# Kernel tuning notes

Measured on AMD Instinct MI355X. Metric: run time of the kernel, lower is better.

Reference implementation:

```python
import jax, jax.numpy as jnp
import numpy as np

NUM_HEADS = 16
HEAD_DIM = 64
LORA_SCALE = 1.0 / 8.0  # lora_alpha (1) / r (8), loralib defaults


def setup_inputs() -> dict:
    key = jax.random.key(0)
    ks = jax.random.split(key, 10)
    B, N, C = 4, 2048, 1024
    O = 3 * NUM_HEADS * HEAD_DIM  # 3072
    s = lambda fan: 1.0 / np.sqrt(fan)
    return {
        "x": jax.random.normal(ks[0], (B, N, C), jnp.float32),
        "W_qkv": jax.random.normal(ks[1], (O, C), jnp.float32) * s(C),
        "W_lora": jax.random.normal(ks[2], (O, C), jnp.float32) * s(C),
        "b_lora": jax.random.normal(ks[3], (O,), jnp.float32) * s(C),
        "A_q": jax.random.normal(ks[4], (8, C), jnp.float32) * s(C),
        "B_q": jnp.zeros((NUM_HEADS * HEAD_DIM, 8), jnp.float32) + jax.random.normal(ks[5], (NUM_HEADS * HEAD_DIM, 8), jnp.float32) * 0.02,
        "A_v": jax.random.normal(ks[6], (8, C), jnp.float32) * s(C),
        "B_v": jax.random.normal(ks[7], (NUM_HEADS * HEAD_DIM, 8), jnp.float32) * 0.02,
        "W_out": jax.random.normal(ks[8], (C, NUM_HEADS * HEAD_DIM), jnp.float32) * s(NUM_HEADS * HEAD_DIM),
        "b_out": jax.random.normal(ks[9], (C,), jnp.float32) * s(NUM_HEADS * HEAD_DIM),
    }


def reference(x, W_qkv, W_lora, b_lora, A_q, B_q, A_v, B_v, W_out, b_out):
    B, N, C = x.shape
    H, D = NUM_HEADS, HEAD_DIM
    scale = D ** (-0.5)

    def split_qkv(t):
        t = t.reshape(B, N, 3, H, D).transpose(2, 0, 3, 1, 4)
        return t[0], t[1], t[2]

    q, k, v = split_qkv(jnp.einsum('bnc,oc->bno', x, W_qkv))
    ql, _, vl = split_qkv(jnp.einsum('bnc,oc->bno', x, W_lora) + b_lora)

    # low-rank LoRA updates for Q and V slices only (K disabled)
    dq = (jnp.einsum('bnc,rc->bnr', x, A_q) @ B_q.T) * LORA_SCALE  # (B,N,HD)
    dv = (jnp.einsum('bnc,rc->bnr', x, A_v) @ B_v.T) * LORA_SCALE
    dq = dq.reshape(B, N, H, D).transpose(0, 2, 1, 3)
    dv = dv.reshape(B, N, H, D).transpose(0, 2, 1, 3)

    q = q + ql + dq
    v = v + vl + dv

    attn = jax.nn.softmax(jnp.einsum('bhnd,bhmd->bhnm', q, k) * scale, axis=-1)
    out = jnp.einsum('bhnm,bhmd->bhnd', attn, v)
    out = out.transpose(0, 2, 1, 3).reshape(B, N, H * D)  # b h n d -> b n (h d)
    return jnp.einsum('bnk,ck->bnc', out, W_out) + b_out
```

## Files before the change

### kernel.cpp

```cpp
#include <hip/hip_runtime.h>
#include <hip/hip_bf16.h>

typedef unsigned short u16;
typedef unsigned int u32;
typedef __attribute__((ext_vector_type(8))) short bf16x8;
typedef __attribute__((ext_vector_type(4))) float f32x4;

#define GLDS16(gptr, lptr)                                                        \
  __builtin_amdgcn_global_load_lds(                                               \
      (__attribute__((address_space(1))) const void*)(gptr),                      \
      (__attribute__((address_space(3))) void*)(lptr), 16, 0, 0)

__device__ __forceinline__ u16 f2bf(float f) {
  union { float f; unsigned u; } v; v.f = f;
  unsigned r = v.u + 0x7fffu + ((v.u >> 16) & 1u);
  return (u16)(r >> 16);
}

__device__ __forceinline__ u32 pack_bf2(float a, float b) {
  union { __hip_bfloat162 h2; u32 u; } v;
  v.h2 = __float22bfloat162_rn(make_float2(a, b));
  return v.u;
}

__global__ void k_f32_to_bf16(const float* __restrict__ in, u16* __restrict__ out, int n4) {
  int i = blockIdx.x * 256 + threadIdx.x;
  if (i < n4) {
    float4 f = reinterpret_cast<const float4*>(in)[i];
    ushort4 u;
    u.x = f2bf(f.x); u.y = f2bf(f.y); u.z = f2bf(f.z); u.w = f2bf(f.w);
    reinterpret_cast<ushort4*>(out)[i] = u;
  }
}

__global__ void k_prep_weff(const float* __restrict__ Wqkv, const float* __restrict__ Wlora,
                            const float* __restrict__ blora,
                            const float* __restrict__ Aq, const float* __restrict__ Bq,
                            const float* __restrict__ Av, const float* __restrict__ Bv,
                            u16* __restrict__ Weff, float* __restrict__ beff) {
  int idx = blockIdx.x * 256 + threadIdx.x;
  int o = idx >> 10, c = idx & 1023;
  float w = Wqkv[idx];
  if (o < 1024) {
    float lr = 0.f;
#pragma unroll
    for (int r = 0; r < 8; ++r) lr += Bq[o * 8 + r] * Aq[r * 1024 + c];
    w += Wlora[idx] + 0.125f * lr;
  } else if (o >= 2048) {
    int o2 = o - 2048;
    float lr = 0.f;
#pragma unroll
    for (int r = 0; r < 8; ++r) lr += Bv[o2 * 8 + r] * Av[r * 1024 + c];
    w += Wlora[idx] + 0.125f * lr;
  }
  Weff[idx] = f2bf(w);
  if (c == 0) beff[o] = (o < 1024 || o >= 2048) ? blora[o] : 0.f;
}

__global__ __launch_bounds__(256, 2)
void k_gemm_qkv(const u16* __restrict__ Xb, const u16* __restrict__ Weff,
                const float* __restrict__ beff, u16* __restrict__ Y, u16* __restrict__ Vt) {
  __shared__ u16 As[128 * 32], Bs[128 * 32];
  const int tid = threadIdx.x, lane = tid & 63, wave = tid >> 6;
  const int lr = lane & 15, lg = lane >> 4;
  const int wr = wave >> 1, wc = wave & 1;
  const int m0 = blockIdx.y * 128, n0 = blockIdx.x * 128;
  f32x4 acc[4][4] = {};

  for (int k0 = 0; k0 < 1024; k0 += 32) {
#pragma unroll
    for (int i = 0; i < 2; ++i) {
      int gc = ((tid & 3) ^ ((tid >> 2) & 3)) << 3;
      GLDS16(Xb + (size_t)(m0 + i * 64 + (tid >> 2)) * 1024 + k0 + gc, As + i * 2048 + wave * 512);
      GLDS16(Weff + (size_t)(n0 + i * 64 + (tid >> 2)) * 1024 + k0 + gc, Bs + i * 2048 + wave * 512);
    }
    __syncthreads();
    bf16x8 af[4], bfr[4];
#pragma unroll
    for (int t = 0; t < 4; ++t) {
      int ch = ((lg ^ (lr & 3)) & 3) << 3;
      af[t]  = *reinterpret_cast<const bf16x8*>(As + (wr * 64 + t * 16 + lr) * 32 + ch);
      bfr[t] = *reinterpret_cast<const bf16x8*>(Bs + (wc * 64 + t * 16 + lr) * 32 + ch);
    }
#pragma unroll
    for (int mi = 0; mi < 4; ++mi)
#pragma unroll
      for (int ni = 0; ni < 4; ++ni)
        acc[mi][ni] = __builtin_amdgcn_mfma_f32_16x16x32_bf16(af[mi], bfr[ni], acc[mi][ni], 0, 0, 0);
    __syncthreads();
  }

#pragma unroll
  for (int mi = 0; mi < 4; ++mi) {
    int row = m0 + wr * 64 + mi * 16 + (lg << 2);
#pragma unroll
    for (int ni = 0; ni < 4; ++ni) {
      int col = n0 + wc * 64 + ni * 16 + lr;
      float bias = beff[col];
      float vs[4];
#pragma unroll
      for (int j = 0; j < 4; ++j) {
        float v = acc[mi][ni][j] + bias;
        if (col < 1024) v *= 0.125f;
        vs[j] = v;
        Y[(size_t)(row + j) * 3072 + col] = f2bf(v);
      }
      if (col >= 2048) {
        int hd = col - 2048;
        int bb = row >> 11, n = row & 2047;
        ushort4 pk;
        pk.x = f2bf(vs[0]); pk.y = f2bf(vs[1]); pk.z = f2bf(vs[2]); pk.w = f2bf(vs[3]);
        *reinterpret_cast<ushort4*>(Vt + (size_t)(bb * 1024 + hd) * 2048 + n) = pk;
      }
    }
  }
}

__global__ __launch_bounds__(256, 3)
void k_attn(const u16* __restrict__ Y, const u16* __restrict__ Vt, u16* __restrict__ Oa) {
  __shared__ u16 Ks[64 * 64], Vs[64 * 64];
  __shared__ u32 Pp[4 * 16 * 32];
  const int tid = threadIdx.x, lane = tid & 63, wave = tid >> 6;
  const int b = blockIdx.y >> 4, h = blockIdx.y & 15;
  const int q0 = blockIdx.x * 128;
  const int lr = lane & 15, lg = lane >> 4;

  bf16x8 qa[2][2];
#pragma unroll
  for (int g = 0; g < 2; ++g) {
    size_t row = (size_t)(b * 2048 + q0 + wave * 32 + g * 16 + lr);
#pragma unroll
    for (int hf = 0; hf < 2; ++hf)
      qa[g][hf] = *reinterpret_cast<const bf16x8*>(Y + row * 3072 + h * 64 + hf * 32 + lg * 8);
  }

  float m_run[2] = {-1e30f, -1e30f}, l_run[2] = {0.f, 0.f};
  f32x4 oacc[2][4] = {};

  const int sr = tid >> 3, sc = tid & 7;
  const u32 pbase = wave * 512 + lr * 32;
  const u32 pswz  = (lr & 7) << 4;

  for (int kt = 0; kt < 32; ++kt) {
    const int key0 = kt * 64;
#pragma unroll
    for (int i = 0; i < 2; ++i) {
      int r = i * 32 + sr;
      int gc = (sc ^ (r & 7)) << 3;
      GLDS16(Y + (size_t)(b * 2048 + key0 + r) * 3072 + 1024 + h * 64 + gc, Ks + i * 2048 + wave * 512);
      GLDS16(Vt + (size_t)(b * 1024 + h * 64 + r) * 2048 + key0 + gc,       Vs + i * 2048 + wave * 512);
    }
    __syncthreads();

    bf16x8 kb[4][2], vb[4][2];
#pragma unroll
    for (int s = 0; s < 4; ++s) {
      int row = s * 16 + lr;
#pragma unroll
      for (int hf = 0; hf < 2; ++hf) {
        int ch = ((hf * 4 + lg) ^ (row & 7)) << 3;
        kb[s][hf] = *reinterpret_cast<const bf16x8*>(Ks + row * 64 + ch);
        vb[s][hf] = *reinterpret_cast<const bf16x8*>(Vs + row * 64 + ch);
      }
    }

#pragma unroll
    for (int g = 0; g < 2; ++g) {
      f32x4 p4[4] = {};
      __builtin_amdgcn_s_setprio(1);
#pragma unroll
      for (int s = 0; s < 4; ++s)
#pragma unroll
        for (int hf = 0; hf < 2; ++hf)
          p4[s] = __builtin_amdgcn_mfma_f32_16x16x32_bf16(kb[s][hf], qa[g][hf], p4[s], 0, 0, 0);
      __builtin_amdgcn_s_setprio(0);

      float tmax = fmaxf(fmaxf(p4[0][0], p4[0][1]), fmaxf(p4[0][2], p4[0][3]));
#pragma unroll
      for (int s = 1; s < 4; ++s)
        tmax = fmaxf(tmax, fmaxf(fmaxf(p4[s][0], p4[s][1]), fmaxf(p4[s][2], p4[s][3])));
      tmax = fmaxf(tmax, __shfl_xor(tmax, 16));
      tmax = fmaxf(tmax, __shfl_xor(tmax, 32));

      if (__any(tmax > m_run[g] + 8.f)) {
        float mnew = fmaxf(m_run[g], tmax);
        float alpha = __expf(m_run[g] - mnew);
        m_run[g] = mnew;
        l_run[g] *= alpha;
        float abc[4];
#pragma unroll
        for (int j = 0; j < 4; ++j) abc[j] = __shfl(alpha, (lg << 2) + j);
#pragma unroll
        for (int dt = 0; dt < 4; ++dt)
#pragma unroll
          for (int j = 0; j < 4; ++j) oacc[g][dt][j] *= abc[j];
      }

      float rs = 0.f;
      u32 w[4][2];
#pragma unroll
      for (int s = 0; s < 4; ++s) {
        float e0 = __expf(p4[s][0] - m_run[g]);
        float e1 = __expf(p4[s][1] - m_run[g]);
        float e2 = __expf(p4[s][2] - m_run[g]);
        float e3 = __expf(p4[s][3] - m_run[g]);
        rs += (e0 + e1) + (e2 + e3);
        w[s][0] = pack_bf2(e0, e1);
        w[s][1] = pack_bf2(e2, e3);
      }
      rs += __shfl_xor(rs, 16);
      rs += __shfl_xor(rs, 32);
      l_run[g] += rs;

#pragma unroll
      for (int s = 0; s < 4; ++s) {
        u32 ui = pbase + ((((u32)(s * 32 + lg * 8)) ^ pswz) >> 2);
        *reinterpret_cast<uint2*>(&Pp[ui]) = make_uint2(w[s][0], w[s][1]);
      }
      asm volatile("s_waitcnt lgkmcnt(0)" ::: "memory");
      __builtin_amdgcn_sched_barrier(0);

      __builtin_amdgcn_s_setprio(1);
#pragma unroll
      for (int kk = 0; kk < 2; ++kk) {
        u32 ur = pbase + ((((u32)(kk * 64 + lg * 16)) ^ pswz) >> 2);
        bf16x8 pa = *reinterpret_cast<const bf16x8*>(&Pp[ur]);
#pragma unroll
        for (int dt = 0; dt < 4; ++dt)
          oacc[g][dt] = __builtin_amdgcn_mfma_f32_16x16x32_bf16(pa, vb[dt][kk], oacc[g][dt], 0, 0, 0);
      }
      __builtin_amdgcn_s_setprio(0);
    }
    __syncthreads();
  }

#pragma unroll
  for (int g = 0; g < 2; ++g) {
    float lbc[4];
#pragma unroll
    for (int j = 0; j < 4; ++j)
      lbc[j] = __builtin_amdgcn_rcpf(__shfl(l_run[g], (lg << 2) + j));
    int rowb = b * 2048 + q0 + wave * 32 + g * 16 + (lg << 2);
#pragma unroll
    for (int dt = 0; dt < 4; ++dt) {
      int col = h * 64 + dt * 16 + lr;
#pragma unroll
      for (int j = 0; j < 4; ++j) {
        float v = oacc[g][dt][j] * lbc[j];
        Oa[(size_t)(rowb + j) * 1024 + col] = f2bf(v);
      }
    }
  }
}

__global__ __launch_bounds__(256, 2)
void k_gemm_out(const u16* __restrict__ Ob, const u16* __restrict__ Wb,
                const float* __restrict__ bout, float* __restrict__ out) {
  __shared__ u16 As[128 * 32], Bs[128 * 32];
  const int tid = threadIdx.x, lane = tid & 63, wave = tid >> 6;
  const int lr = lane & 15, lg = lane >> 4;
  const int wr = wave >> 1, wc = wave & 1;
  const int m0 = blockIdx.y * 128, n0 = blockIdx.x * 128;
  f32x4 acc[4][4] = {};

  for (int k0 = 0; k0 < 1024; k0 += 32) {
#pragma unroll
    for (int i = 0; i < 2; ++i) {
      int gc = ((tid & 3) ^ ((tid >> 2) & 3)) << 3;
      GLDS16(Ob + (size_t)(m0 + i * 64 + (tid >> 2)) * 1024 + k0 + gc, As + i * 2048 + wave * 512);
      GLDS16(Wb + (size_t)(n0 + i * 64 + (tid >> 2)) * 1024 + k0 + gc, Bs + i * 2048 + wave * 512);
    }
    __syncthreads();
    bf16x8 af[4], bfr[4];
#pragma unroll
    for (int t = 0; t < 4; ++t) {
      int ch = ((lg ^ (lr & 3)) & 3) << 3;
      af[t]  = *reinterpret_cast<const bf16x8*>(As + (wr * 64 + t * 16 + lr) * 32 + ch);
      bfr[t] = *reinterpret_cast<const bf16x8*>(Bs + (wc * 64 + t * 16 + lr) * 32 + ch);
    }
#pragma unroll
    for (int mi = 0; mi < 4; ++mi)
#pragma unroll
      for (int ni = 0; ni < 4; ++ni)
        acc[mi][ni] = __builtin_amdgcn_mfma_f32_16x16x32_bf16(af[mi], bfr[ni], acc[mi][ni], 0, 0, 0);
    __syncthreads();
  }

#pragma unroll
  for (int mi = 0; mi < 4; ++mi) {
    int row = m0 + wr * 64 + mi * 16 + (lg << 2);
#pragma unroll
    for (int ni = 0; ni < 4; ++ni) {
      int col = n0 + wc * 64 + ni * 16 + lr;
      float bias = bout[col];
#pragma unroll
      for (int j = 0; j < 4; ++j)
        out[(size_t)(row + j) * 1024 + col] = acc[mi][ni][j] + bias;
    }
  }
}

extern "C" void kernel_launch(void* const* d_in, const int* in_sizes, int n_in,
                              void* d_out, int out_size, void* d_ws, size_t ws_size,
                              hipStream_t stream) {
  const float* x     = (const float*)d_in[0];
  const float* Wqkv  = (const float*)d_in[1];
  const float* Wlora = (const float*)d_in[2];
  const float* blora = (const float*)d_in[3];
  const float* Aq    = (const float*)d_in[4];
  const float* Bq    = (const float*)d_in[5];
  const float* Av    = (const float*)d_in[6];
  const float* Bv    = (const float*)d_in[7];
  const float* Wout  = (const float*)d_in[8];
  const float* bout  = (const float*)d_in[9];
  float* out = (float*)d_out;

  char* w = (char*)d_ws;
  auto alloc = [&](size_t bytes) { char* p = w; w += (bytes + 255) & ~(size_t)255; return p; };
  u16*   Xb    = (u16*)alloc((size_t)8192 * 1024 * 2);
  u16*   Weff  = (u16*)alloc((size_t)3072 * 1024 * 2);
  float* beff  = (float*)alloc((size_t)3072 * 4);
  u16*   Woutb = (u16*)alloc((size_t)1024 * 1024 * 2);
  u16*   Y     = (u16*)alloc((size_t)8192 * 3072 * 2);
  u16*   Vt    = (u16*)alloc((size_t)4096 * 1024 * 2 * 2);
  u16*   Oa    = Xb;

  k_f32_to_bf16<<<dim3(8192), dim3(256), 0, stream>>>(x, Xb, 8192 * 1024 / 4);
  k_f32_to_bf16<<<dim3(1024), dim3(256), 0, stream>>>(Wout, Woutb, 1024 * 1024 / 4);
  k_prep_weff<<<dim3(12288), dim3(256), 0, stream>>>(Wqkv, Wlora, blora, Aq, Bq, Av, Bv, Weff, beff);
  k_gemm_qkv<<<dim3(24, 64), dim3(256), 0, stream>>>(Xb, Weff, beff, Y, Vt);
  k_attn<<<dim3(16, 64), dim3(256), 0, stream>>>(Y, Vt, Oa);
  k_gemm_out<<<dim3(8, 64), dim3(256), 0, stream>>>(Oa, Woutb, bout, out);
}
```

Measured before the change: 354.4 us.

## Double-buffer attention K/V tiles, use exp2 softmax, move V transpose to own kernel

```diff
diff --git a/kernel.cpp b/kernel.cpp
--- a/kernel.cpp
+++ b/kernel.cpp
@@ -59,7 +59,7 @@
 
 __global__ __launch_bounds__(256, 2)
 void k_gemm_qkv(const u16* __restrict__ Xb, const u16* __restrict__ Weff,
-                const float* __restrict__ beff, u16* __restrict__ Y, u16* __restrict__ Vt) {
+                const float* __restrict__ beff, u16* __restrict__ Y) {
   __shared__ u16 As[128 * 32], Bs[128 * 32];
   const int tid = threadIdx.x, lane = tid & 63, wave = tid >> 6;
   const int lr = lane & 15, lg = lane >> 4;
@@ -97,41 +97,62 @@
     for (int ni = 0; ni < 4; ++ni) {
       int col = n0 + wc * 64 + ni * 16 + lr;
       float bias = beff[col];
-      float vs[4];
 #pragma unroll
       for (int j = 0; j < 4; ++j) {
         float v = acc[mi][ni][j] + bias;
-        if (col < 1024) v *= 0.125f;
-        vs[j] = v;
+        if (col < 1024) v *= 0.18033688011112042f;
         Y[(size_t)(row + j) * 3072 + col] = f2bf(v);
       }
-      if (col >= 2048) {
-        int hd = col - 2048;
-        int bb = row >> 11, n = row & 2047;
-        ushort4 pk;
-        pk.x = f2bf(vs[0]); pk.y = f2bf(vs[1]); pk.z = f2bf(vs[2]); pk.w = f2bf(vs[3]);
-        *reinterpret_cast<ushort4*>(Vt + (size_t)(bb * 1024 + hd) * 2048 + n) = pk;
-      }
-    }
+    }
+  }
+}
+
+__global__ __launch_bounds__(256)
+void k_vtrans(const u16* __restrict__ Y, u16* __restrict__ Vt) {
+  __shared__ u16 Ls[64 * 65];
+  const int t = threadIdx.x;
+  const int bh = blockIdx.y, b = bh >> 4, h = bh & 15;
+  const int n0 = blockIdx.x * 64;
+#pragma unroll
+  for (int c = 0; c < 2; ++c) {
+    int idx = c * 256 + t;
+    int nl = idx >> 3, d0 = (idx & 7) * 8;
+    bf16x8 val = *reinterpret_cast<const bf16x8*>(
+        Y + (size_t)(b * 2048 + n0 + nl) * 3072 + 2048 + h * 64 + d0);
+#pragma unroll
+    for (int j = 0; j < 8; ++j) Ls[(d0 + j) * 65 + nl] = (u16)val[j];
+  }
+  __syncthreads();
+#pragma unroll
+  for (int c = 0; c < 2; ++c) {
+    int idx = c * 256 + t;
+    int dl = idx >> 3, nn = (idx & 7) * 8;
+    bf16x8 outv;
+#pragma unroll
+    for (int j = 0; j < 8; ++j) outv[j] = (short)Ls[dl * 65 + nn + j];
+    *reinterpret_cast<bf16x8*>(Vt + (size_t)(bh * 64 + dl) * 2048 + n0 + nn) = outv;
   }
 }
 
 __global__ __launch_bounds__(256, 3)
 void k_attn(const u16* __restrict__ Y, const u16* __restrict__ Vt, u16* __restrict__ Oa) {
-  __shared__ u16 Ks[64 * 64], Vs[64 * 64];
+  __shared__ u16 Ks[2][64 * 64], Vs[2][64 * 64];
   __shared__ u32 Pp[4 * 16 * 32];
   const int tid = threadIdx.x, lane = tid & 63, wave = tid >> 6;
   const int b = blockIdx.y >> 4, h = blockIdx.y & 15;
   const int q0 = blockIdx.x * 128;
   const int lr = lane & 15, lg = lane >> 4;
+  const size_t bq = (size_t)b * 2048;
+  const size_t bv = (size_t)b * 1024 + h * 64;
+  const int hc = h * 64;
 
   bf16x8 qa[2][2];
 #pragma unroll
   for (int g = 0; g < 2; ++g) {
-    size_t row = (size_t)(b * 2048 + q0 + wave * 32 + g * 16 + lr);
+    size_t row = bq + q0 + wave * 32 + g * 16 + lr;
 #pragma unroll
     for (int hf = 0; hf < 2; ++hf)
-      qa[g][hf] = *reinterpret_cast<const bf16x8*>(Y + row * 3072 + h * 64 + hf * 32 + lg * 8);
+      qa[g][hf] = *reinterpret_cast<const bf16x8*>(Y + row * 3072 + hc + hf * 32 + lg * 8);
   }
 
   float m_run[2] = {-1e30f, -1e30f}, l_run[2] = {0.f, 0.f};
@@ -141,16 +162,27 @@
   const u32 pbase = wave * 512 + lr * 32;
   const u32 pswz  = (lr & 7) << 4;
 
-  for (int kt = 0; kt < 32; ++kt) {
-    const int key0 = kt * 64;
+  auto stage = [&](int key0, int bb) {
 #pragma unroll
     for (int i = 0; i < 2; ++i) {
       int r = i * 32 + sr;
       int gc = (sc ^ (r & 7)) << 3;
-      GLDS16(Y + (size_t)(b * 2048 + key0 + r) * 3072 + 1024 + h * 64 + gc, Ks + i * 2048 + wave * 512);
-      GLDS16(Vt + (size_t)(b * 1024 + h * 64 + r) * 2048 + key0 + gc,       Vs + i * 2048 + wave * 512);
-    }
-    __syncthreads();
+      GLDS16(Y + (bq + key0 + r) * 3072 + 1024 + hc + gc, &Ks[bb][i * 2048 + wave * 512]);
+      GLDS16(Vt + (bv + r) * 2048 + key0 + gc,            &Vs[bb][i * 2048 + wave * 512]);
+    }
+  };
+
+  stage(0, 0);
+  for (int kt = 0; kt < 32; ++kt) {
+    const int cur = kt & 1;
+    if (kt < 31) {
+      stage((kt + 1) * 64, cur ^ 1);
+      asm volatile("s_waitcnt vmcnt(4)" ::: "memory");
+    } else {
+      asm volatile("s_waitcnt vmcnt(0)" ::: "memory");
+    }
+    __builtin_amdgcn_s_barrier();
+    asm volatile("" ::: "memory");
 
     bf16x8 kb[4][2], vb[4][2];
 #pragma unroll
@@ -159,8 +191,8 @@
 #pragma unroll
       for (int hf = 0; hf < 2; ++hf) {
         int ch = ((hf * 4 + lg) ^ (row & 7)) << 3;
-        kb[s][hf] = *reinterpret_cast<const bf16x8*>(Ks + row * 64 + ch);
-        vb[s][hf] = *reinterpret_cast<const bf16x8*>(Vs + row * 64 + ch);
+        kb[s][hf] = *reinterpret_cast<const bf16x8*>(&Ks[cur][row * 64 + ch]);
+        vb[s][hf] = *reinterpret_cast<const bf16x8*>(&Vs[cur][row * 64 + ch]);
       }
     }
 
@@ -175,16 +207,17 @@
           p4[s] = __builtin_amdgcn_mfma_f32_16x16x32_bf16(kb[s][hf], qa[g][hf], p4[s], 0, 0, 0);
       __builtin_amdgcn_s_setprio(0);
 
-      float tmax = fmaxf(fmaxf(p4[0][0], p4[0][1]), fmaxf(p4[0][2], p4[0][3]));
-#pragma unroll
-      for (int s = 1; s < 4; ++s)
-        tmax = fmaxf(tmax, fmaxf(fmaxf(p4[s][0], p4[s][1]), fmaxf(p4[s][2], p4[s][3])));
+      float ma = fmaxf(fmaxf(p4[0][0], p4[0][1]), fmaxf(p4[0][2], p4[0][3]));
+      float mb = fmaxf(fmaxf(p4[1][0], p4[1][1]), fmaxf(p4[1][2], p4[1][3]));
+      float mc = fmaxf(fmaxf(p4[2][0], p4[2][1]), fmaxf(p4[2][2], p4[2][3]));
+      float md = fmaxf(fmaxf(p4[3][0], p4[3][1]), fmaxf(p4[3][2], p4[3][3]));
+      float tmax = fmaxf(fmaxf(ma, mb), fmaxf(mc, md));
       tmax = fmaxf(tmax, __shfl_xor(tmax, 16));
       tmax = fmaxf(tmax, __shfl_xor(tmax, 32));
 
-      if (__any(tmax > m_run[g] + 8.f)) {
+      if (__any(tmax > m_run[g] + 11.0f)) {
         float mnew = fmaxf(m_run[g], tmax);
-        float alpha = __expf(m_run[g] - mnew);
+        float alpha = __builtin_amdgcn_exp2f(m_run[g] - mnew);
         m_run[g] = mnew;
         l_run[g] *= alpha;
         float abc[4];
@@ -200,10 +233,10 @@
       u32 w[4][2];
 #pragma unroll
       for (int s = 0; s < 4; ++s) {
-        float e0 = __expf(p4[s][0] - m_run[g]);
-        float e1 = __expf(p4[s][1] - m_run[g]);
-        float e2 = __expf(p4[s][2] - m_run[g]);
-        float e3 = __expf(p4[s][3] - m_run[g]);
+        float e0 = __builtin_amdgcn_exp2f(p4[s][0] - m_run[g]);
+        float e1 = __builtin_amdgcn_exp2f(p4[s][1] - m_run[g]);
+        float e2 = __builtin_amdgcn_exp2f(p4[s][2] - m_run[g]);
+        float e3 = __builtin_amdgcn_exp2f(p4[s][3] - m_run[g]);
         rs += (e0 + e1) + (e2 + e3);
         w[s][0] = pack_bf2(e0, e1);
         w[s][1] = pack_bf2(e2, e3);
@@ -231,7 +264,8 @@
       }
       __builtin_amdgcn_s_setprio(0);
     }
-    __syncthreads();
+    asm volatile("" ::: "memory");
+    __builtin_amdgcn_s_barrier();
   }
 
 #pragma unroll
@@ -240,10 +274,10 @@
 #pragma unroll
     for (int j = 0; j < 4; ++j)
       lbc[j] = __builtin_amdgcn_rcpf(__shfl(l_run[g], (lg << 2) + j));
-    int rowb = b * 2048 + q0 + wave * 32 + g * 16 + (lg << 2);
+    int rowb = (int)bq + q0 + wave * 32 + g * 16 + (lg << 2);
 #pragma unroll
     for (int dt = 0; dt < 4; ++dt) {
-      int col = h * 64 + dt * 16 + lr;
+      int col = hc + dt * 16 + lr;
 #pragma unroll
       for (int j = 0; j < 4; ++j) {
         float v = oacc[g][dt][j] * lbc[j];
@@ -328,7 +362,8 @@
   k_f32_to_bf16<<<dim3(8192), dim3(256), 0, stream>>>(x, Xb, 8192 * 1024 / 4);
   k_f32_to_bf16<<<dim3(1024), dim3(256), 0, stream>>>(Wout, Woutb, 1024 * 1024 / 4);
   k_prep_weff<<<dim3(12288), dim3(256), 0, stream>>>(Wqkv, Wlora, blora, Aq, Bq, Av, Bv, Weff, beff);
-  k_gemm_qkv<<<dim3(24, 64), dim3(256), 0, stream>>>(Xb, Weff, beff, Y, Vt);
+  k_gemm_qkv<<<dim3(24, 64), dim3(256), 0, stream>>>(Xb, Weff, beff, Y);
+  k_vtrans<<<dim3(32, 64), dim3(256), 0, stream>>>(Y, Vt);
   k_attn<<<dim3(16, 64), dim3(256), 0, stream>>>(Y, Vt, Oa);
   k_gemm_out<<<dim3(8, 64), dim3(256), 0, stream>>>(Oa, Woutb, bout, out);
 }
```

After: 347.4 us. -2.0%, faster.
